# Kernel tuning notes

Hardware: AMD Instinct MI355X
Metric: run time of the kernel (lower is better)

## Reference

```python
import jax, jax.numpy as jnp
import numpy as np

N = 50000      # nodes
E = 800000     # edges (before self-loops)
G = 256        # graphs in batch
IN = 64        # in_dim
H = 8          # n_heads
C = 16         # gat_dim (per-head out channels)
HID = 128      # decoder hidden
OUT = H * C    # 128 = concat GAT output = graph_embedding_dim
NEG_SLOPE = 0.2


def setup_inputs() -> dict:
    key = jax.random.key(0)
    ks = jax.random.split(key, 12)
    op_features = jax.random.normal(ks[0], (N, IN), dtype=jnp.float32)
    edge_index = jax.random.randint(ks[1], (2, E), 0, N, dtype=jnp.int64)
    batch_index = jnp.sort(jax.random.randint(ks[2], (N,), 0, G, dtype=jnp.int64))
    # GATConv params (PyG: lin weight, att_src, att_dst, bias)
    W_gat = jax.random.normal(ks[3], (IN, H * C), dtype=jnp.float32) / np.sqrt(IN)
    att_src = jax.random.normal(ks[4], (H, C), dtype=jnp.float32) / np.sqrt(C)
    att_dst = jax.random.normal(ks[5], (H, C), dtype=jnp.float32) / np.sqrt(C)
    bias_gat = jnp.zeros((H * C,), dtype=jnp.float32)
    # Decoder MLP: Linear(OUT+OUT, 128) -> ReLU -> Linear(128, 1)
    W1 = jax.random.normal(ks[6], (2 * OUT, HID), dtype=jnp.float32) / np.sqrt(2 * OUT)
    b1 = jnp.zeros((HID,), dtype=jnp.float32)
    W2 = jax.random.normal(ks[7], (HID, 1), dtype=jnp.float32) / np.sqrt(HID)
    b2 = jnp.zeros((1,), dtype=jnp.float32)
    return {
        "op_features": op_features, "edge_index": edge_index, "batch_index": batch_index,
        "W_gat": W_gat, "att_src": att_src, "att_dst": att_dst, "bias_gat": bias_gat,
        "W1": W1, "b1": b1, "W2": W2, "b2": b2,
    }


def _gat_conv(x_in, src, dst, W_gat, att_src, att_dst, bias_gat):
    # x: [N, H, C] transformed node features
    x = (x_in @ W_gat).reshape(N, H, C)
    # per-node attention logits (PyG splits alpha into src+dst halves)
    a_src = jnp.einsum('nhc,hc->nh', x, att_src)   # [N, H]
    a_dst = jnp.einsum('nhc,hc->nh', x, att_dst)   # [N, H]
    # edge logits: message flows src -> dst
    alpha = jax.nn.leaky_relu(a_src[src] + a_dst[dst], NEG_SLOPE)  # [E', H]
    # scatter-softmax over incoming edges of each dst node
    m = jax.ops.segment_max(alpha, dst, num_segments=N)            # [N, H]
    e = jnp.exp(alpha - m[dst])                                    # [E', H]
    s = jax.ops.segment_sum(e, dst, num_segments=N)                # [N, H]
    a = e / s[dst]
    # weighted aggregation of source features
    out = jax.ops.segment_sum(a[:, :, None] * x[src], dst, num_segments=N)  # [N, H, C]
    return out.reshape(N, H * C) + bias_gat


def reference(op_features, edge_index, batch_index, W_gat, att_src, att_dst,
              bias_gat, W1, b1, W2, b2):
    # add self-loops (PyG GATConv default add_self_loops=True)
    loop = jnp.arange(N, dtype=edge_index.dtype)
    src = jnp.concatenate([edge_index[0], loop])
    dst = jnp.concatenate([edge_index[1], loop])

    op_embedding = jax.nn.elu(_gat_conv(op_features, src, dst,
                                        W_gat, att_src, att_dst, bias_gat))  # [N, OUT]
    # global_mean_pool
    sums = jax.ops.segment_sum(op_embedding, batch_index, num_segments=G)    # [G, OUT]
    cnts = jax.ops.segment_sum(jnp.ones((N,), op_embedding.dtype), batch_index, num_segments=G)
    graph_embedding = sums / jnp.maximum(cnts, 1.0)[:, None]
    # gather-broadcast + concat + MLP decoder
    combined = jnp.concatenate([op_embedding, graph_embedding[batch_index]], axis=1)  # [N, 2*OUT]
    h = jax.nn.relu(combined @ W1 + b1)
    scores = (h @ W2 + b2).squeeze(-1)   # [N]
    return scores, graph_embedding
```

## Files before the change

### kernel.cpp

```cpp
#include <hip/hip_runtime.h>
#include <hip/hip_bf16.h>
#include <hip/hip_fp16.h>

constexpr int N_   = 50000;
constexpr int E_   = 800000;
constexpr int G_   = 256;
constexpr int IN_  = 64;
constexpr int H_   = 8;
constexpr int OUT_ = 128;
constexpr float NEG_SLOPE = 0.2f;
constexpr int NBUCK = (N_ + 255) / 256;
constexpr int EPB   = 4096;
constexpr int CAP   = 6144;

typedef _Float16 f16x8 __attribute__((ext_vector_type(8)));
typedef float    f32x4 __attribute__((ext_vector_type(4)));

constexpr size_t OFF_X      = 0;
constexpr size_t OFF_EMBH   = OFF_X      + (size_t)N_*OUT_*2;
constexpr size_t OFF_ASRC   = OFF_X      + (size_t)N_*OUT_*4;
constexpr size_t OFF_ADST   = OFF_ASRC   + (size_t)N_*H_*4;
constexpr size_t OFF_PAIRS  = OFF_ADST   + (size_t)N_*H_*4;
constexpr size_t OFF_GSUM   = OFF_PAIRS  + (size_t)NBUCK*CAP*4;
constexpr size_t OFF_BCNT   = OFF_GSUM   + (size_t)G_*OUT_*4;
constexpr size_t OFF_WT     = OFF_BCNT   + 1024;
constexpr size_t OFF_WP     = OFF_WT     + 128*128*2;
constexpr size_t OFF_BSTART = OFF_WP     + 18432;
constexpr size_t OFF_ROWS   = OFF_BSTART + 1024;
constexpr size_t OFF_EIDX   = OFF_ROWS   + 200448;
constexpr size_t OFF_GPART  = OFF_EIDX   + (size_t)E_*4;
constexpr size_t ZERO_BEG   = OFF_GSUM;
constexpr size_t ZERO_LEN   = OFF_WT - OFF_GSUM;

__global__ void k_prep(const float* __restrict__ Wg, const float* __restrict__ att_s,
                       const float* __restrict__ att_d, const float* __restrict__ W1,
                       __half* __restrict__ wp, __half* __restrict__ wt) {
    const int b = blockIdx.x, t = threadIdx.x;
    if (b == 0) {
        for (int idx = t; idx < 16 * 64; idx += 256) {
            int jp = idx >> 6, k = idx & 63;
            int h = jp & 7;
            const float* att = (jp < 8) ? att_s : att_d;
            float s = 0.f;
#pragma unroll
            for (int c = 0; c < 16; ++c)
                s = fmaf(Wg[k * 128 + h * 16 + c], att[h * 16 + c], s);
            wp[(128 + jp) * 64 + k] = __float2half(s);
        }
    } else if (b <= 8) {
        for (int idx = t; idx < 1024; idx += 256) {
            int e = (b - 1) * 1024 + idx;
            int j = e >> 6, k = e & 63;
            wp[j * 64 + k] = __float2half(Wg[k * 128 + j]);
        }
    } else {
        for (int idx = t; idx < 2048; idx += 256) {
            int e = (b - 9) * 2048 + idx;
            int j = e >> 7, k = e & 127;
            wt[j * 128 + k] = __float2half(W1[(size_t)k * 128 + j]);
        }
    }
}

__global__ __launch_bounds__(256) void k_xform(const float* __restrict__ feat,
                                               const __half* __restrict__ wp,
                                               __half* __restrict__ xh,
                                               float* __restrict__ asrc,
                                               float* __restrict__ adst) {
    __shared__ _Float16 fs[64][64];
    __shared__ _Float16 wp_s[144][64];
    const int base = blockIdx.x * 64;
    const int tid  = threadIdx.x;

    for (int c = tid; c < 1152; c += 256) {
        int j = c >> 3, kk = (c & 7) * 8;
        *(float4*)&wp_s[j][kk] = *(const float4*)&wp[j * 64 + kk];
    }
    for (int c = tid; c < 512; c += 256) {
        int nl = c >> 3, kk = (c & 7) * 8;
        int n = base + nl;
        _Float16 h8[8];
        if (n < N_) {
            float4 f0 = *(const float4*)&feat[(size_t)n * 64 + kk];
            float4 f1 = *(const float4*)&feat[(size_t)n * 64 + kk + 4];
            h8[0]=(_Float16)f0.x; h8[1]=(_Float16)f0.y; h8[2]=(_Float16)f0.z; h8[3]=(_Float16)f0.w;
            h8[4]=(_Float16)f1.x; h8[5]=(_Float16)f1.y; h8[6]=(_Float16)f1.z; h8[7]=(_Float16)f1.w;
        } else {
#pragma unroll
            for (int q = 0; q < 8; ++q) h8[q] = (_Float16)0.f;
        }
        *(float4*)&fs[nl][kk] = *(float4*)h8;
    }
    __syncthreads();

    const int wv   = tid >> 6;
    const int lane = tid & 63;
    const int rc   = lane & 15;
    const int kh   = lane >> 4;

    f32x4 acc[9];
#pragma unroll
    for (int nt = 0; nt < 9; ++nt) acc[nt] = (f32x4){0.f, 0.f, 0.f, 0.f};

#pragma unroll
    for (int kt = 0; kt < 2; ++kt) {
        f16x8 a = *(const f16x8*)&fs[wv * 16 + rc][kt * 32 + kh * 8];
#pragma unroll
        for (int nt = 0; nt < 9; ++nt) {
            f16x8 bfr = *(const f16x8*)&wp_s[nt * 16 + rc][kt * 32 + kh * 8];
            acc[nt] = __builtin_amdgcn_mfma_f32_16x16x32_f16(a, bfr, acc[nt], 0, 0, 0);
        }
    }

#pragma unroll
    for (int r = 0; r < 4; ++r) {
        int n = base + wv * 16 + kh * 4 + r;
        if (n >= N_) continue;
#pragma unroll
        for (int nt = 0; nt < 8; ++nt)
            xh[(size_t)n * OUT_ + nt * 16 + rc] = __float2half(acc[nt][r]);
        if (rc < 8) asrc[n * H_ + rc] = acc[8][r];
        else        adst[n * H_ + (rc - 8)] = acc[8][r];
    }
}

__global__ __launch_bounds__(256) void k_bin(const int* __restrict__ src,
                                             const int* __restrict__ dst,
                                             int* __restrict__ bcnt,
                                             unsigned int* __restrict__ pairs) {
    __shared__ int cnt[NBUCK];
    __shared__ int base[NBUCK];
    const int tid = threadIdx.x;
    for (int i = tid; i < NBUCK; i += 256) cnt[i] = 0;
    __syncthreads();
    const int e0 = blockIdx.x * EPB;
    const int ne = min(EPB, E_ - e0);
    for (int i = tid; i < ne; i += 256) atomicAdd(&cnt[dst[e0 + i] >> 8], 1);
    __syncthreads();
    for (int i = tid; i < NBUCK; i += 256) {
        int c = cnt[i];
        base[i] = (c > 0) ? atomicAdd(&bcnt[i], c) : 0;
        cnt[i] = 0;
    }
    __syncthreads();
    for (int i = tid; i < ne; i += 256) {
        int d = dst[e0 + i];
        int s = src[e0 + i];
        int b = d >> 8;
        int p = base[b] + atomicAdd(&cnt[b], 1);
        pairs[(size_t)b * CAP + p] = ((unsigned int)(d & 255) << 16) | (unsigned int)s;
    }
}

__global__ void k_scanb(const int* __restrict__ bcnt, int* __restrict__ bstart) {
    __shared__ int s[256];
    int t = threadIdx.x;
    int v = (t < NBUCK) ? bcnt[t] : 0;
    s[t] = v;
    __syncthreads();
    for (int off = 1; off < 256; off <<= 1) {
        int u = (t >= off) ? s[t - off] : 0;
        __syncthreads();
        s[t] += u;
        __syncthreads();
    }
    if (t < NBUCK) bstart[t] = s[t] - v;
    if (t == NBUCK - 1) bstart[NBUCK] = s[t];
}

__global__ __launch_bounds__(256) void k_scat3(const unsigned int* __restrict__ pairs,
                                               const int* __restrict__ bcnt,
                                               const int* __restrict__ bstart,
                                               int* __restrict__ rowstart,
                                               int* __restrict__ eidx) {
    __shared__ int cnt[256];
    __shared__ int s[256];
    __shared__ int cur[256];
    const int b  = blockIdx.x;
    const int t  = threadIdx.x;
    const int nb = bcnt[b];
    const size_t p0 = (size_t)b * CAP;

    cnt[t] = 0;
    __syncthreads();
    for (int i = t; i < nb; i += 256)
        atomicAdd(&cnt[pairs[p0 + i] >> 16], 1);
    __syncthreads();
    int v = cnt[t];
    s[t] = v;
    __syncthreads();
    for (int off = 1; off < 256; off <<= 1) {
        int u = (t >= off) ? s[t - off] : 0;
        __syncthreads();
        s[t] += u;
        __syncthreads();
    }
    int rs = bstart[b] + s[t] - v;
    int n = b * 256 + t;
    if (n < N_) rowstart[n] = rs;
    if (b == NBUCK - 1 && t == 0) rowstart[N_] = E_;
    cur[t] = rs;
    __syncthreads();
    for (int i = t; i < nb; i += 256) {
        unsigned int pk = pairs[p0 + i];
        int d = (int)(pk >> 16);
        int pos = atomicAdd(&cur[d], 1);
        eidx[pos] = (int)(pk & 0xFFFFu);
    }
}

__global__ void k_agg(const int* __restrict__ rowstart, const int* __restrict__ eidx,
                      const __half* __restrict__ xh, const float* __restrict__ asrc,
                      const float* __restrict__ adst, const float* __restrict__ bias,
                      __half* __restrict__ embh) {
    const int dn   = blockIdx.x * 4 + (threadIdx.x >> 6);
    const int lane = threadIdx.x & 63;
    const int h    = lane >> 3;
    const float adst_h = adst[dn * H_ + h];
    const uint choff = (uint)lane * 2;

    const int beg = rowstart[dn];
    const int end = rowstart[dn + 1];

    float ax = 0.f, ay = 0.f, sw = 0.f;
    int i = beg;
    for (; i + 3 < end; i += 4) {
        int s0 = eidx[i];
        int s1 = eidx[i + 1];
        int s2 = eidx[i + 2];
        int s3 = eidx[i + 3];
        __half2 x0 = *(const __half2*)(xh + ((uint)s0 * OUT_ + choff));
        __half2 x1 = *(const __half2*)(xh + ((uint)s1 * OUT_ + choff));
        __half2 x2 = *(const __half2*)(xh + ((uint)s2 * OUT_ + choff));
        __half2 x3 = *(const __half2*)(xh + ((uint)s3 * OUT_ + choff));
        float a0 = asrc[(uint)s0 * H_ + h] + adst_h;
        float a1 = asrc[(uint)s1 * H_ + h] + adst_h;
        float a2 = asrc[(uint)s2 * H_ + h] + adst_h;
        float a3 = asrc[(uint)s3 * H_ + h] + adst_h;
        a0 = (a0 > 0.f) ? a0 : NEG_SLOPE * a0;
        a1 = (a1 > 0.f) ? a1 : NEG_SLOPE * a1;
        a2 = (a2 > 0.f) ? a2 : NEG_SLOPE * a2;
        a3 = (a3 > 0.f) ? a3 : NEG_SLOPE * a3;
        float w0 = __expf(a0);
        float w1 = __expf(a1);
        float w2 = __expf(a2);
        float w3 = __expf(a3);
        float2 f0 = __half22float2(x0);
        float2 f1 = __half22float2(x1);
        float2 f2 = __half22float2(x2);
        float2 f3 = __half22float2(x3);
        ax = fmaf(w0, f0.x, fmaf(w1, f1.x, fmaf(w2, f2.x, fmaf(w3, f3.x, ax))));
        ay = fmaf(w0, f0.y, fmaf(w1, f1.y, fmaf(w2, f2.y, fmaf(w3, f3.y, ay))));
        sw += (w0 + w1) + (w2 + w3);
    }
    for (; i < end; ++i) {
        int s0 = eidx[i];
        __half2 x0 = *(const __half2*)(xh + ((uint)s0 * OUT_ + choff));
        float a0 = asrc[(uint)s0 * H_ + h] + adst_h;
        a0 = (a0 > 0.f) ? a0 : NEG_SLOPE * a0;
        float w0 = __expf(a0);
        float2 f0 = __half22float2(x0);
        ax = fmaf(w0, f0.x, ax);
        ay = fmaf(w0, f0.y, ay);
        sw += w0;
    }
    {
        float al = asrc[(uint)dn * H_ + h] + adst_h;
        al = (al > 0.f) ? al : NEG_SLOPE * al;
        float w = __expf(al);
        __half2 xv = *(const __half2*)(xh + ((uint)dn * OUT_ + choff));
        float2 fv = __half22float2(xv);
        ax = fmaf(w, fv.x, ax);
        ay = fmaf(w, fv.y, ay);
        sw += w;
    }
    float ox = ax / sw + bias[lane * 2];
    float oy = ay / sw + bias[lane * 2 + 1];
    ox = (ox > 0.f) ? ox : expm1f(ox);
    oy = (oy > 0.f) ? oy : expm1f(oy);
    *(__half2*)&embh[(size_t)dn * OUT_ + lane * 2] = __floats2half2_rn(ox, oy);
}

__global__ void k_pool(const __half* __restrict__ embh, const int* __restrict__ batch,
                       float* __restrict__ gsum) {
    int c   = threadIdx.x & 63;
    int grp = threadIdx.x >> 6;
    int base = blockIdx.x * 64 + grp * 16;
    float rx = 0.f, ry = 0.f;
    int gcur = -1;
    for (int i = 0; i < 16; ++i) {
        int n = base + i;
        if (n >= N_) break;
        int g = batch[n];
        if (g != gcur) {
            if (gcur >= 0) {
                unsafeAtomicAdd(&gsum[gcur * OUT_ + 2 * c], rx);
                unsafeAtomicAdd(&gsum[gcur * OUT_ + 2 * c + 1], ry);
            }
            gcur = g; rx = ry = 0.f;
        }
        __half2 v = *(const __half2*)&embh[(size_t)n * OUT_ + 2 * c];
        float2 f = __half22float2(v);
        rx += f.x; ry += f.y;
    }
    if (gcur >= 0) {
        unsafeAtomicAdd(&gsum[gcur * OUT_ + 2 * c], rx);
        unsafeAtomicAdd(&gsum[gcur * OUT_ + 2 * c + 1], ry);
    }
}

__global__ void k_graph(const int* __restrict__ batch, const float* __restrict__ gsum,
                        const float* __restrict__ W1, const float* __restrict__ b1,
                        float* __restrict__ outg, float* __restrict__ gpart) {
    const int g = blockIdx.x;
    const int j = threadIdx.x;
    __shared__ float ge[128];
    __shared__ int cnt_s;
    if (j == 0) {
        int lo = 0, hi = N_;
        while (lo < hi) { int m = (lo + hi) >> 1; if (batch[m] < g) lo = m + 1; else hi = m; }
        int start = lo;
        lo = 0; hi = N_;
        while (lo < hi) { int m = (lo + hi) >> 1; if (batch[m] <= g) lo = m + 1; else hi = m; }
        cnt_s = lo - start;
    }
    __syncthreads();
    float v = gsum[g * 128 + j] / fmaxf((float)cnt_s, 1.f);
    ge[j] = v;
    outg[g * 128 + j] = v;
    __syncthreads();
    float s = b1[j];
    const float* w = W1 + (size_t)128 * 128 + j;
    for (int k = 0; k < 128; ++k) s = fmaf(ge[k], w[(size_t)k * 128], s);
    gpart[g * 128 + j] = s;
}

__global__ __launch_bounds__(256) void k_dec3(const __half* __restrict__ embh,
                                              const __half* __restrict__ wtg,
                                              const float* __restrict__ gpart,
                                              const int* __restrict__ batch,
                                              const float* __restrict__ W2,
                                              const float* __restrict__ b2,
                                              float* __restrict__ scores) {
    __shared__ _Float16 wt_s[128][128];
    __shared__ _Float16 emb_s[64][128];
    __shared__ float    w2_s[128];
    const int base = blockIdx.x * 64;
    const int tid  = threadIdx.x;

    for (int c = tid; c < 2048; c += 256) {
        int j = c >> 4, kk = (c & 15) * 8;
        *(float4*)&wt_s[j][kk] = *(const float4*)&wtg[j * 128 + kk];
    }
    for (int c = tid; c < 1024; c += 256) {
        int nl = c >> 4, kk = (c & 15) * 8;
        int n = base + nl;
        if (n < N_)
            *(float4*)&emb_s[nl][kk] = *(const float4*)&embh[(size_t)n * 128 + kk];
        else
            *(float4*)&emb_s[nl][kk] = make_float4(0.f, 0.f, 0.f, 0.f);
    }
    if (tid < 128) w2_s[tid] = W2[tid];
    __syncthreads();

    const int wv   = tid >> 6;
    const int lane = tid & 63;
    const int rc   = lane & 15;
    const int kh   = lane >> 4;

    f32x4 acc[8];
#pragma unroll
    for (int nt = 0; nt < 8; ++nt) acc[nt] = (f32x4){0.f, 0.f, 0.f, 0.f};

#pragma unroll
    for (int kt = 0; kt < 4; ++kt) {
        f16x8 a = *(const f16x8*)&emb_s[wv * 16 + rc][kt * 32 + kh * 8];
#pragma unroll
        for (int nt = 0; nt < 8; ++nt) {
            f16x8 bfr = *(const f16x8*)&wt_s[nt * 16 + rc][kt * 32 + kh * 8];
            acc[nt] = __builtin_amdgcn_mfma_f32_16x16x32_f16(a, bfr, acc[nt], 0, 0, 0);
        }
    }

    const float b2v = b2[0];
    float s[4] = {0.f, 0.f, 0.f, 0.f};
    int   gi[4];
#pragma unroll
    for (int r = 0; r < 4; ++r) {
        int n = base + wv * 16 + kh * 4 + r;
        gi[r] = (n < N_) ? batch[n] : 0;
    }
#pragma unroll
    for (int nt = 0; nt < 8; ++nt) {
        int j = nt * 16 + rc;
        float w2 = w2_s[j];
#pragma unroll
        for (int r = 0; r < 4; ++r) {
            float hv = acc[nt][r] + gpart[(size_t)gi[r] * 128 + j];
            hv = (hv > 0.f) ? hv : 0.f;
            s[r] = fmaf(hv, w2, s[r]);
        }
    }
#pragma unroll
    for (int r = 0; r < 4; ++r) {
#pragma unroll
        for (int m = 8; m >= 1; m >>= 1) s[r] += __shfl_xor(s[r], m, 16);
    }
    if (rc == 0) {
#pragma unroll
        for (int r = 0; r < 4; ++r) {
            int n = base + wv * 16 + kh * 4 + r;
            if (n < N_) scores[n] = s[r] + b2v;
        }
    }
}

extern "C" void kernel_launch(void* const* d_in, const int* in_sizes, int n_in,
                              void* d_out, int out_size, void* d_ws, size_t ws_size,
                              hipStream_t stream) {
    const float* feat   = (const float*)d_in[0];
    const int*   ei     = (const int*)d_in[1];
    const int*   batch  = (const int*)d_in[2];
    const float* Wg     = (const float*)d_in[3];
    const float* att_s  = (const float*)d_in[4];
    const float* att_d  = (const float*)d_in[5];
    const float* bias_g = (const float*)d_in[6];
    const float* W1     = (const float*)d_in[7];
    const float* b1     = (const float*)d_in[8];
    const float* W2     = (const float*)d_in[9];
    const float* b2     = (const float*)d_in[10];
    char*  wsb = (char*)d_ws;
    float* out = (float*)d_out;

    const int* src = ei;
    const int* dst = ei + E_;

    __half* XH    = (__half*)(wsb + OFF_X);
    __half* EMBH  = (__half*)(wsb + OFF_EMBH);
    float*  ASRC  = (float*)(wsb + OFF_ASRC);
    float*  ADST  = (float*)(wsb + OFF_ADST);
    unsigned int* PAIRS = (unsigned int*)(wsb + OFF_PAIRS);
    float*  GSUM  = (float*)(wsb + OFF_GSUM);
    int*    BCNT  = (int*)  (wsb + OFF_BCNT);
    __half* WT    = (__half*)(wsb + OFF_WT);
    __half* WP    = (__half*)(wsb + OFF_WP);
    int*    BSTART= (int*)  (wsb + OFF_BSTART);
    int*    ROWS  = (int*)  (wsb + OFF_ROWS);
    int*    EIDX  = (int*)  (wsb + OFF_EIDX);
    float*  GPART = (float*)(wsb + OFF_GPART);

    hipMemsetAsync(wsb + ZERO_BEG, 0, ZERO_LEN, stream);

    k_prep<<<17, 256, 0, stream>>>(Wg, att_s, att_d, W1, WP, WT);
    k_bin<<<(E_ + EPB - 1) / EPB, 256, 0, stream>>>(src, dst, BCNT, PAIRS);
    k_scanb<<<1, 256, 0, stream>>>(BCNT, BSTART);
    k_scat3<<<NBUCK, 256, 0, stream>>>(PAIRS, BCNT, BSTART, ROWS, EIDX);
    k_xform<<<(N_ + 63) / 64, 256, 0, stream>>>(feat, WP, XH, ASRC, ADST);
    k_agg<<<N_ / 4, 256, 0, stream>>>(ROWS, EIDX, XH, ASRC, ADST, bias_g, EMBH);
    k_pool<<<(N_ + 63) / 64, 256, 0, stream>>>(EMBH, batch, GSUM);
    k_graph<<<G_, 128, 0, stream>>>(batch, GSUM, W1, b1, out + N_, GPART);
    k_dec3<<<(N_ + 63) / 64, 256, 0, stream>>>(EMBH, WT, GPART, batch, W2, b2, out);
}
```

Baseline: 134.4 us.

## Merge launch chain: fuse binning with transform, scan into scatter, pool into graph

```diff
diff --git a/kernel.cpp b/kernel.cpp
--- a/kernel.cpp
+++ b/kernel.cpp
@@ -11,7 +11,9 @@
 constexpr float NEG_SLOPE = 0.2f;
 constexpr int NBUCK = (N_ + 255) / 256;
 constexpr int EPB   = 4096;
+constexpr int NBINB = (E_ + EPB - 1) / EPB;
 constexpr int CAP   = 6144;
+constexpr int NXF   = (N_ + 63) / 64;
 
 typedef _Float16 f16x8 __attribute__((ext_vector_type(8)));
 typedef float    f32x4 __attribute__((ext_vector_type(4)));
@@ -21,22 +23,20 @@
 constexpr size_t OFF_ASRC   = OFF_X      + (size_t)N_*OUT_*4;
 constexpr size_t OFF_ADST   = OFF_ASRC   + (size_t)N_*H_*4;
 constexpr size_t OFF_PAIRS  = OFF_ADST   + (size_t)N_*H_*4;
-constexpr size_t OFF_GSUM   = OFF_PAIRS  + (size_t)NBUCK*CAP*4;
-constexpr size_t OFF_BCNT   = OFF_GSUM   + (size_t)G_*OUT_*4;
+constexpr size_t OFF_BCNT   = OFF_PAIRS  + (size_t)NBUCK*CAP*4;
 constexpr size_t OFF_WT     = OFF_BCNT   + 1024;
 constexpr size_t OFF_WP     = OFF_WT     + 128*128*2;
-constexpr size_t OFF_BSTART = OFF_WP     + 18432;
-constexpr size_t OFF_ROWS   = OFF_BSTART + 1024;
+constexpr size_t OFF_ROWS   = OFF_WP     + 18432;
 constexpr size_t OFF_EIDX   = OFF_ROWS   + 200448;
 constexpr size_t OFF_GPART  = OFF_EIDX   + (size_t)E_*4;
-constexpr size_t ZERO_BEG   = OFF_GSUM;
-constexpr size_t ZERO_LEN   = OFF_WT - OFF_GSUM;
 
 __global__ void k_prep(const float* __restrict__ Wg, const float* __restrict__ att_s,
                        const float* __restrict__ att_d, const float* __restrict__ W1,
-                       __half* __restrict__ wp, __half* __restrict__ wt) {
+                       __half* __restrict__ wp, __half* __restrict__ wt,
+                       int* __restrict__ bcnt) {
     const int b = blockIdx.x, t = threadIdx.x;
     if (b == 0) {
+        for (int i = t; i < NBUCK; i += 256) bcnt[i] = 0;
         for (int idx = t; idx < 16 * 64; idx += 256) {
             int jp = idx >> 6, k = idx & 63;
             int h = jp & 7;
@@ -62,19 +62,51 @@
     }
 }
 
-__global__ __launch_bounds__(256) void k_xform(const float* __restrict__ feat,
-                                               const __half* __restrict__ wp,
-                                               __half* __restrict__ xh,
-                                               float* __restrict__ asrc,
-                                               float* __restrict__ adst) {
-    __shared__ _Float16 fs[64][64];
-    __shared__ _Float16 wp_s[144][64];
-    const int base = blockIdx.x * 64;
-    const int tid  = threadIdx.x;
-
+__global__ __launch_bounds__(256) void k_binx(const int* __restrict__ src,
+                                              const int* __restrict__ dst,
+                                              int* __restrict__ bcnt,
+                                              unsigned int* __restrict__ pairs,
+                                              const float* __restrict__ feat,
+                                              const __half* __restrict__ wp,
+                                              __half* __restrict__ xh,
+                                              float* __restrict__ asrc,
+                                              float* __restrict__ adst) {
+    union SMem {
+        struct { int cnt[NBUCK]; int base[NBUCK]; } bin;
+        struct { _Float16 fs[64][64]; _Float16 wp_s[144][64]; } xf;
+    };
+    __shared__ SMem sm;
+    const int tid = threadIdx.x;
+
+    if (blockIdx.x < NBINB) {
+        int* cnt  = sm.bin.cnt;
+        int* base = sm.bin.base;
+        for (int i = tid; i < NBUCK; i += 256) cnt[i] = 0;
+        __syncthreads();
+        const int e0 = blockIdx.x * EPB;
+        const int ne = min(EPB, E_ - e0);
+        for (int i = tid; i < ne; i += 256) atomicAdd(&cnt[dst[e0 + i] >> 8], 1);
+        __syncthreads();
+        for (int i = tid; i < NBUCK; i += 256) {
+            int c = cnt[i];
+            base[i] = (c > 0) ? atomicAdd(&bcnt[i], c) : 0;
+            cnt[i] = 0;
+        }
+        __syncthreads();
+        for (int i = tid; i < ne; i += 256) {
+            int d = dst[e0 + i];
+            int s = src[e0 + i];
+            int b = d >> 8;
+            int p = base[b] + atomicAdd(&cnt[b], 1);
+            pairs[(size_t)b * CAP + p] = ((unsigned int)(d & 255) << 16) | (unsigned int)s;
+        }
+        return;
+    }
+
+    const int base = (blockIdx.x - NBINB) * 64;
     for (int c = tid; c < 1152; c += 256) {
         int j = c >> 3, kk = (c & 7) * 8;
-        *(float4*)&wp_s[j][kk] = *(const float4*)&wp[j * 64 + kk];
+        *(float4*)&sm.xf.wp_s[j][kk] = *(const float4*)&wp[j * 64 + kk];
     }
     for (int c = tid; c < 512; c += 256) {
         int nl = c >> 3, kk = (c & 7) * 8;
@@ -89,7 +121,7 @@
 #pragma unroll
             for (int q = 0; q < 8; ++q) h8[q] = (_Float16)0.f;
         }
-        *(float4*)&fs[nl][kk] = *(float4*)h8;
+        *(float4*)&sm.xf.fs[nl][kk] = *(float4*)h8;
     }
     __syncthreads();
 
@@ -104,10 +136,10 @@
 
 #pragma unroll
     for (int kt = 0; kt < 2; ++kt) {
-        f16x8 a = *(const f16x8*)&fs[wv * 16 + rc][kt * 32 + kh * 8];
+        f16x8 a = *(const f16x8*)&sm.xf.fs[wv * 16 + rc][kt * 32 + kh * 8];
 #pragma unroll
         for (int nt = 0; nt < 9; ++nt) {
-            f16x8 bfr = *(const f16x8*)&wp_s[nt * 16 + rc][kt * 32 + kh * 8];
+            f16x8 bfr = *(const f16x8*)&sm.xf.wp_s[nt * 16 + rc][kt * 32 + kh * 8];
             acc[nt] = __builtin_amdgcn_mfma_f32_16x16x32_f16(a, bfr, acc[nt], 0, 0, 0);
         }
     }
@@ -124,78 +156,45 @@
     }
 }
 
-__global__ __launch_bounds__(256) void k_bin(const int* __restrict__ src,
-                                             const int* __restrict__ dst,
-                                             int* __restrict__ bcnt,
-                                             unsigned int* __restrict__ pairs) {
-    __shared__ int cnt[NBUCK];
-    __shared__ int base[NBUCK];
-    const int tid = threadIdx.x;
-    for (int i = tid; i < NBUCK; i += 256) cnt[i] = 0;
-    __syncthreads();
-    const int e0 = blockIdx.x * EPB;
-    const int ne = min(EPB, E_ - e0);
-    for (int i = tid; i < ne; i += 256) atomicAdd(&cnt[dst[e0 + i] >> 8], 1);
-    __syncthreads();
-    for (int i = tid; i < NBUCK; i += 256) {
-        int c = cnt[i];
-        base[i] = (c > 0) ? atomicAdd(&bcnt[i], c) : 0;
-        cnt[i] = 0;
-    }
-    __syncthreads();
-    for (int i = tid; i < ne; i += 256) {
-        int d = dst[e0 + i];
-        int s = src[e0 + i];
-        int b = d >> 8;
-        int p = base[b] + atomicAdd(&cnt[b], 1);
-        pairs[(size_t)b * CAP + p] = ((unsigned int)(d & 255) << 16) | (unsigned int)s;
-    }
-}
-
-__global__ void k_scanb(const int* __restrict__ bcnt, int* __restrict__ bstart) {
-    __shared__ int s[256];
-    int t = threadIdx.x;
-    int v = (t < NBUCK) ? bcnt[t] : 0;
-    s[t] = v;
-    __syncthreads();
-    for (int off = 1; off < 256; off <<= 1) {
-        int u = (t >= off) ? s[t - off] : 0;
-        __syncthreads();
-        s[t] += u;
-        __syncthreads();
-    }
-    if (t < NBUCK) bstart[t] = s[t] - v;
-    if (t == NBUCK - 1) bstart[NBUCK] = s[t];
-}
-
 __global__ __launch_bounds__(256) void k_scat3(const unsigned int* __restrict__ pairs,
                                                const int* __restrict__ bcnt,
-                                               const int* __restrict__ bstart,
                                                int* __restrict__ rowstart,
                                                int* __restrict__ eidx) {
+    __shared__ int sh[256];
     __shared__ int cnt[256];
-    __shared__ int s[256];
     __shared__ int cur[256];
-    const int b  = blockIdx.x;
-    const int t  = threadIdx.x;
+    const int b = blockIdx.x;
+    const int t = threadIdx.x;
+
+    int v0 = (t < NBUCK) ? bcnt[t] : 0;
+    sh[t] = v0;
+    __syncthreads();
+    for (int off = 1; off < 256; off <<= 1) {
+        int u = (t >= off) ? sh[t - off] : 0;
+        __syncthreads();
+        sh[t] += u;
+        __syncthreads();
+    }
+    const int bstart_b = (b == 0) ? 0 : sh[b - 1];
     const int nb = bcnt[b];
+    __syncthreads();
+
+    cnt[t] = 0;
+    __syncthreads();
     const size_t p0 = (size_t)b * CAP;
-
-    cnt[t] = 0;
-    __syncthreads();
     for (int i = t; i < nb; i += 256)
         atomicAdd(&cnt[pairs[p0 + i] >> 16], 1);
     __syncthreads();
     int v = cnt[t];
-    s[t] = v;
+    sh[t] = v;
     __syncthreads();
     for (int off = 1; off < 256; off <<= 1) {
-        int u = (t >= off) ? s[t - off] : 0;
-        __syncthreads();
-        s[t] += u;
-        __syncthreads();
-    }
-    int rs = bstart[b] + s[t] - v;
+        int u = (t >= off) ? sh[t - off] : 0;
+        __syncthreads();
+        sh[t] += u;
+        __syncthreads();
+    }
+    int rs = bstart_b + sh[t] - v;
     int n = b * 256 + t;
     if (n < N_) rowstart[n] = rs;
     if (b == NBUCK - 1 && t == 0) rowstart[N_] = E_;
@@ -203,8 +202,7 @@
     __syncthreads();
     for (int i = t; i < nb; i += 256) {
         unsigned int pk = pairs[p0 + i];
-        int d = (int)(pk >> 16);
-        int pos = atomicAdd(&cur[d], 1);
+        int pos = atomicAdd(&cur[pk >> 16], 1);
         eidx[pos] = (int)(pk & 0xFFFFu);
     }
 }
@@ -281,51 +279,24 @@
     *(__half2*)&embh[(size_t)dn * OUT_ + lane * 2] = __floats2half2_rn(ox, oy);
 }
 
-__global__ void k_pool(const __half* __restrict__ embh, const int* __restrict__ batch,
-                       float* __restrict__ gsum) {
-    int c   = threadIdx.x & 63;
-    int grp = threadIdx.x >> 6;
-    int base = blockIdx.x * 64 + grp * 16;
-    float rx = 0.f, ry = 0.f;
-    int gcur = -1;
-    for (int i = 0; i < 16; ++i) {
-        int n = base + i;
-        if (n >= N_) break;
-        int g = batch[n];
-        if (g != gcur) {
-            if (gcur >= 0) {
-                unsafeAtomicAdd(&gsum[gcur * OUT_ + 2 * c], rx);
-                unsafeAtomicAdd(&gsum[gcur * OUT_ + 2 * c + 1], ry);
-            }
-            gcur = g; rx = ry = 0.f;
-        }
-        __half2 v = *(const __half2*)&embh[(size_t)n * OUT_ + 2 * c];
-        float2 f = __half22float2(v);
-        rx += f.x; ry += f.y;
-    }
-    if (gcur >= 0) {
-        unsafeAtomicAdd(&gsum[gcur * OUT_ + 2 * c], rx);
-        unsafeAtomicAdd(&gsum[gcur * OUT_ + 2 * c + 1], ry);
-    }
-}
-
-__global__ void k_graph(const int* __restrict__ batch, const float* __restrict__ gsum,
-                        const float* __restrict__ W1, const float* __restrict__ b1,
-                        float* __restrict__ outg, float* __restrict__ gpart) {
+__global__ void k_pg(const __half* __restrict__ embh, const int* __restrict__ batch,
+                     const float* __restrict__ W1, const float* __restrict__ b1,
+                     float* __restrict__ outg, float* __restrict__ gpart) {
     const int g = blockIdx.x;
     const int j = threadIdx.x;
+    int lo = 0, hi = N_;
+    while (lo < hi) { int m = (lo + hi) >> 1; if (batch[m] < g) lo = m + 1; else hi = m; }
+    const int start = lo;
+    hi = N_;
+    while (lo < hi) { int m = (lo + hi) >> 1; if (batch[m] <= g) lo = m + 1; else hi = m; }
+    const int end = lo;
+
+    float acc = 0.f;
+    for (int n = start; n < end; ++n)
+        acc += __half2float(embh[(size_t)n * OUT_ + j]);
+    float v = acc / fmaxf((float)(end - start), 1.f);
+
     __shared__ float ge[128];
-    __shared__ int cnt_s;
-    if (j == 0) {
-        int lo = 0, hi = N_;
-        while (lo < hi) { int m = (lo + hi) >> 1; if (batch[m] < g) lo = m + 1; else hi = m; }
-        int start = lo;
-        lo = 0; hi = N_;
-        while (lo < hi) { int m = (lo + hi) >> 1; if (batch[m] <= g) lo = m + 1; else hi = m; }
-        cnt_s = lo - start;
-    }
-    __syncthreads();
-    float v = gsum[g * 128 + j] / fmaxf((float)cnt_s, 1.f);
     ge[j] = v;
     outg[g * 128 + j] = v;
     __syncthreads();
@@ -440,24 +411,18 @@
     float*  ASRC  = (float*)(wsb + OFF_ASRC);
     float*  ADST  = (float*)(wsb + OFF_ADST);
     unsigned int* PAIRS = (unsigned int*)(wsb + OFF_PAIRS);
-    float*  GSUM  = (float*)(wsb + OFF_GSUM);
     int*    BCNT  = (int*)  (wsb + OFF_BCNT);
     __half* WT    = (__half*)(wsb + OFF_WT);
     __half* WP    = (__half*)(wsb + OFF_WP);
-    int*    BSTART= (int*)  (wsb + OFF_BSTART);
     int*    ROWS  = (int*)  (wsb + OFF_ROWS);
     int*    EIDX  = (int*)  (wsb + OFF_EIDX);
     float*  GPART = (float*)(wsb + OFF_GPART);
 
-    hipMemsetAsync(wsb + ZERO_BEG, 0, ZERO_LEN, stream);
-
-    k_prep<<<17, 256, 0, stream>>>(Wg, att_s, att_d, W1, WP, WT);
-    k_bin<<<(E_ + EPB - 1) / EPB, 256, 0, stream>>>(src, dst, BCNT, PAIRS);
-    k_scanb<<<1, 256, 0, stream>>>(BCNT, BSTART);
-    k_scat3<<<NBUCK, 256, 0, stream>>>(PAIRS, BCNT, BSTART, ROWS, EIDX);
-    k_xform<<<(N_ + 63) / 64, 256, 0, stream>>>(feat, WP, XH, ASRC, ADST);
+    k_prep<<<17, 256, 0, stream>>>(Wg, att_s, att_d, W1, WP, WT, BCNT);
+    k_binx<<<NBINB + NXF, 256, 0, stream>>>(src, dst, BCNT, PAIRS,
+                                            feat, WP, XH, ASRC, ADST);
+    k_scat3<<<NBUCK, 256, 0, stream>>>(PAIRS, BCNT, ROWS, EIDX);
     k_agg<<<N_ / 4, 256, 0, stream>>>(ROWS, EIDX, XH, ASRC, ADST, bias_g, EMBH);
-    k_pool<<<(N_ + 63) / 64, 256, 0, stream>>>(EMBH, batch, GSUM);
-    k_graph<<<G_, 128, 0, stream>>>(batch, GSUM, W1, b1, out + N_, GPART);
+    k_pg<<<G_, 128, 0, stream>>>(EMBH, batch, W1, b1, out + N_, GPART);
     k_dec3<<<(N_ + 63) / 64, 256, 0, stream>>>(EMBH, WT, GPART, batch, W2, b2, out);
 }
```

Result: slower. 170.0 us (+26.5%).
